# Optimization experiments

Hardware: AMD Instinct MI355X
Metric: run time of the kernel (lower is better)

Reference implementation:

```python
import jax, jax.numpy as jnp
import numpy as np

B, N, C = 8, 4096, 768
H, M = 12, 64          # num_heads, num_landmarks
D = C // H             # head_dim = 64


def setup_inputs() -> dict:
    key = jax.random.key(0)
    k1, k2, k3, k4 = jax.random.split(key, 4)
    s = 0.02
    return {
        "x": jax.random.normal(k1, (B, N, C), dtype=jnp.float32),
        "w_qkv": jax.random.normal(k2, (3 * C, C), dtype=jnp.float32) * s,
        "w_proj": jax.random.normal(k3, (C, C), dtype=jnp.float32) * s,
        "b_proj": jax.random.normal(k4, (C,), dtype=jnp.float32) * s,
    }


def iterative_inv(mat, n_iter=6):
    # mat: [B, H, M, M]; Newton-Schulz cubic iteration for pseudo-inverse
    I = jnp.eye(mat.shape[-1], dtype=mat.dtype)
    K = mat
    # init: K^T / max_j(sum_i K_ij)  per (B,H)
    scale = jnp.max(jnp.sum(K, axis=-2), axis=-1)[:, :, None, None]
    V = jnp.swapaxes(K, -1, -2) / scale
    for _ in range(n_iter):
        KV = K @ V
        V = 0.25 * V @ (13.0 * I - KV @ (15.0 * I - KV @ (7.0 * I - KV)))
    return V


def reference(x, w_qkv, w_proj, b_proj):
    b, n, c = x.shape
    qkv = (x @ w_qkv.T).reshape(b, n, 3, H, D).transpose(2, 0, 3, 1, 4)  # [3,B,H,N,D]
    Q, K, V = qkv[0], qkv[1], qkv[2]
    Q = Q / (D ** 0.5)
    # landmark pooling (N % M == 0 path): segment means of length N//M
    Kl = K.reshape(b, H, M, n // M, D).mean(axis=-2)  # [B,H,M,D]
    Ql = Q.reshape(b, H, M, n // M, D).mean(axis=-2)  # [B,H,M,D]
    kernel1 = jax.nn.softmax(jnp.einsum('bhnd,bhmd->bhnm', Q, Kl), axis=-1)   # [B,H,N,M]
    kernel2 = jax.nn.softmax(jnp.einsum('bhmd,bhld->bhml', Ql, Kl), axis=-1)  # [B,H,M,M]
    kernel3 = jax.nn.softmax(jnp.einsum('bhmd,bhnd->bhmn', Ql, K), axis=-1)   # [B,H,M,N]
    SV = (kernel1 @ iterative_inv(kernel2)) @ (kernel3 @ V)  # [B,H,N,D]
    SV = SV.transpose(0, 2, 1, 3).reshape(b, n, c)
    out = SV @ w_proj.T + b_proj
    out = out + V.transpose(0, 2, 1, 3).reshape(b, n, c)
    return out
```

## Files before the change

### kernel.cpp

```cpp
#include <hip/hip_runtime.h>
#include <hip/hip_bf16.h>
#include <stdint.h>

typedef __bf16 bf16;
typedef __bf16 bf16x8 __attribute__((ext_vector_type(8)));
typedef __bf16 bf16x4 __attribute__((ext_vector_type(4)));
typedef float f32x4 __attribute__((ext_vector_type(4)));

#define B_ 8
#define N_ 4096
#define C_ 768
#define H_ 12
#define M_ 64
#define D_ 64
#define NT_ 32768
#define C3_ 2304

typedef __attribute__((address_space(3))) void lds_void_t;
typedef const __attribute__((address_space(1))) void gvoid_t;

__device__ __forceinline__ void gl_lds16(const void* gsrc, void* ldst) {
  __builtin_amdgcn_global_load_lds((gvoid_t*)(uintptr_t)gsrc,
                                   (lds_void_t*)(uintptr_t)ldst, 16, 0, 0);
}

__device__ __forceinline__ f32x4 mfma16(bf16x8 a, bf16x8 b, f32x4 c) {
  return __builtin_amdgcn_mfma_f32_16x16x32_bf16(a, b, c, 0, 0, 0);
}

__global__ void k_cvt(const float* __restrict__ in, bf16* __restrict__ out, int n4) {
  const int stride = gridDim.x * blockDim.x;
  for (int i = blockIdx.x * blockDim.x + threadIdx.x; i < n4; i += stride) {
    f32x4 v = *(const f32x4*)(in + (size_t)i * 4);
    bf16x4 o;
    o[0] = (bf16)v[0]; o[1] = (bf16)v[1]; o[2] = (bf16)v[2]; o[3] = (bf16)v[3];
    *(bf16x4*)(out + (size_t)i * 4) = o;
  }
}

__global__ __launch_bounds__(256, 2) void k_qkv(
    const bf16* __restrict__ xbf, const bf16* __restrict__ wbf,
    bf16* __restrict__ Qb, bf16* __restrict__ Kb, bf16* __restrict__ Vb,
    float* __restrict__ Qlf, float* __restrict__ Klf)
{
  __shared__ bf16 As[2][128 * 32];
  __shared__ bf16 Bs[2][128 * 32];
  const int t = threadIdx.x;
  const int wave = t >> 6, lane = t & 63;
  const int bt = blockIdx.x & 255;
  const int ct = blockIdx.x >> 8;
  const int row0 = bt * 128, col0 = ct * 128;
  const int srow = t >> 2;
  const int scol = (t & 3) * 8;
  const bf16* ga = xbf + (size_t)row0 * C_ + scol;
  const bf16* gb = wbf + (size_t)col0 * C_ + scol;
  const int wr = wave >> 1, wc = wave & 1;

  f32x4 acc[4][4] = {};

#define QKV_STAGE(bi, k0)                                                      \
  {                                                                            \
    gl_lds16(ga + (size_t)srow * C_ + (k0), &As[bi][t * 8]);                   \
    gl_lds16(ga + (size_t)(srow + 64) * C_ + (k0), &As[bi][(t + 256) * 8]);    \
    gl_lds16(gb + (size_t)srow * C_ + (k0), &Bs[bi][t * 8]);                   \
    gl_lds16(gb + (size_t)(srow + 64) * C_ + (k0), &Bs[bi][(t + 256) * 8]);    \
  }

  QKV_STAGE(0, 0);
  __syncthreads();
  for (int ks = 0; ks < 24; ++ks) {
    const int buf = ks & 1;
    if (ks < 23) QKV_STAGE(buf ^ 1, (ks + 1) * 32);
    bf16x8 af[4], bfr[4];
#pragma unroll
    for (int i = 0; i < 4; ++i) {
      af[i]  = *(const bf16x8*)&As[buf][(wr * 64 + i * 16 + (lane & 15)) * 32 + 8 * (lane >> 4)];
      bfr[i] = *(const bf16x8*)&Bs[buf][(wc * 64 + i * 16 + (lane & 15)) * 32 + 8 * (lane >> 4)];
    }
#pragma unroll
    for (int i = 0; i < 4; ++i)
#pragma unroll
      for (int j = 0; j < 4; ++j)
        acc[i][j] = mfma16(af[i], bfr[j], acc[i][j]);
    __syncthreads();
  }
#undef QKV_STAGE

  const int colblock = col0 + wc * 64;
  const int which = colblock / C_;
  const int h = (colblock % C_) / D_;
  const int b = row0 >> 12;
  const int n_base = (row0 & (N_ - 1)) + wr * 64;
  bf16* dst = (which == 0) ? Qb : (which == 1) ? Kb : Vb;
  const float scale = (which == 0) ? 0.125f : 1.0f;
  const size_t base = ((size_t)(b * H_ + h) * N_ + n_base) * D_;
#pragma unroll
  for (int i = 0; i < 4; ++i)
#pragma unroll
    for (int q = 0; q < 4; ++q) {
      const int rloc = i * 16 + (lane >> 4) * 4 + q;
#pragma unroll
      for (int j = 0; j < 4; ++j) {
        const int d = j * 16 + (lane & 15);
        dst[base + (size_t)rloc * D_ + d] = (bf16)(acc[i][j][q] * scale);
      }
    }
  if (which < 2) {
    float* lmout = (which == 0) ? Qlf : Klf;
    const int m = n_base >> 6;
#pragma unroll
    for (int j = 0; j < 4; ++j) {
      float s = 0.f;
#pragma unroll
      for (int i = 0; i < 4; ++i)
#pragma unroll
        for (int q = 0; q < 4; ++q) s += acc[i][j][q];
      s *= scale;
      s += __shfl_xor(s, 16);
      s += __shfl_xor(s, 32);
      if ((lane >> 4) == 0)
        lmout[((size_t)(b * H_ + h) * M_ + m) * D_ + j * 16 + lane] = s * (1.0f / 64.0f);
    }
  }
}

__global__ __launch_bounds__(512, 1) void k_inv(
    const float* __restrict__ Qlf, const float* __restrict__ Klf,
    float* __restrict__ pinv)
{
  __shared__ float K2[4096];
  __shared__ float Vm[4096];
  __shared__ float KV[4096];
  __shared__ float T1[4096];
  __shared__ float U1[4096];
  __shared__ float tmp64[64];
  __shared__ float sscale;
  const int t = threadIdx.x;
  const int bh = blockIdx.x;
  const size_t off = (size_t)bh * 4096;
  for (int idx = t; idx < 4096; idx += 512) T1[idx] = Qlf[off + idx];
  for (int idx = t; idx < 4096; idx += 512) {
    const int r = idx >> 6, c = idx & 63;
    U1[c * 64 + r] = Klf[off + idx];
  }
  __syncthreads();
  const int j0 = (t & 15) * 4;
  const int i0 = (t >> 4) * 2;

  auto MMstep = [&](const float* A, const float* Bm, float* O, float dg, float sg, float al) {
    float r2[2][4] = {};
    for (int k = 0; k < 64; ++k) {
      f32x4 bv = *(const f32x4*)&Bm[k * 64 + j0];
      const float a0 = A[(i0 + 0) * 64 + k];
      const float a1 = A[(i0 + 1) * 64 + k];
#pragma unroll
      for (int jj = 0; jj < 4; ++jj) { r2[0][jj] += a0 * bv[jj]; r2[1][jj] += a1 * bv[jj]; }
    }
#pragma unroll
    for (int ii = 0; ii < 2; ++ii)
#pragma unroll
      for (int jj = 0; jj < 4; ++jj)
        O[(i0 + ii) * 64 + j0 + jj] = al * (dg * A[(i0 + ii) * 64 + (j0 + jj)] + sg * r2[ii][jj]);
    __syncthreads();
  };

  {
    float r2[2][4] = {};
    for (int k = 0; k < 64; ++k) {
      f32x4 bv = *(const f32x4*)&U1[k * 64 + j0];
      const float a0 = T1[(i0 + 0) * 64 + k];
      const float a1 = T1[(i0 + 1) * 64 + k];
#pragma unroll
      for (int jj = 0; jj < 4; ++jj) { r2[0][jj] += a0 * bv[jj]; r2[1][jj] += a1 * bv[jj]; }
    }
#pragma unroll
    for (int ii = 0; ii < 2; ++ii)
#pragma unroll
      for (int jj = 0; jj < 4; ++jj)
        K2[(i0 + ii) * 64 + j0 + jj] = __expf(r2[ii][jj]);
  }
  __syncthreads();
  if (t < 64) {
    float s = 0.f;
    for (int k = 0; k < 64; ++k) s += K2[t * 64 + k];
    tmp64[t] = 1.0f / s;
  }
  __syncthreads();
  for (int idx = t; idx < 4096; idx += 512) K2[idx] *= tmp64[idx >> 6];
  __syncthreads();
  if (t < 64) {
    float s = 0.f;
    for (int i = 0; i < 64; ++i) s += K2[i * 64 + t];
    tmp64[t] = s;
  }
  __syncthreads();
  if (t == 0) {
    float mx = tmp64[0];
    for (int j2 = 1; j2 < 64; ++j2) mx = fmaxf(mx, tmp64[j2]);
    sscale = 1.0f / mx;
  }
  __syncthreads();
  for (int idx = t; idx < 4096; idx += 512) {
    const int r = idx >> 6, c = idx & 63;
    Vm[idx] = K2[c * 64 + r] * sscale;
  }
  __syncthreads();

  float* pV = Vm;
  float* pT = T1;
  for (int it = 0; it < 6; ++it) {
    MMstep(K2, pV, KV, 0.f, 1.f, 1.f);
    MMstep(KV, KV, pT, 7.f, -1.f, 1.f);
    MMstep(KV, pT, U1, 15.f, -1.f, 1.f);
    MMstep(pV, U1, pT, 13.f, -1.f, 0.25f);
    float* sw = pV; pV = pT; pT = sw;
  }
  for (int idx = t; idx < 4096; idx += 512) pinv[off + idx] = pV[idx];
}

__global__ __launch_bounds__(256, 2) void k_k3v(
    const bf16* __restrict__ Qlb, const bf16* __restrict__ Kb, const bf16* __restrict__ Vb,
    float* __restrict__ Zacc, float* __restrict__ rowsum_g)
{
  __shared__ bf16 Qls[64 * 64];
  __shared__ bf16 Ks[128 * 64];
  __shared__ bf16 Vs[128 * 64];
  __shared__ bf16 Ps[64 * 128];
  __shared__ float rs[64];
  const int t = threadIdx.x, wave = t >> 6, lane = t & 63;
  const int bh = blockIdx.x >> 3;
  const int chunk = blockIdx.x & 7;
  const size_t kvbase = (size_t)bh * N_ * D_ + (size_t)chunk * 512 * D_;
  {
    const bf16* g = Qlb + (size_t)bh * 4096;
    gl_lds16(g + t * 8, &Qls[t * 8]);
    gl_lds16(g + (t + 256) * 8, &Qls[(t + 256) * 8]);
  }
  if (t < 64) rs[t] = 0.f;
  f32x4 z[4] = {};
  for (int st = 0; st < 4; ++st) {
    const bf16* gk = Kb + kvbase + (size_t)st * 128 * D_;
    const bf16* gv = Vb + kvbase + (size_t)st * 128 * D_;
#pragma unroll
    for (int c = 0; c < 4; ++c) {
      gl_lds16(gk + (t + c * 256) * 8, &Ks[(t + c * 256) * 8]);
      gl_lds16(gv + (t + c * 256) * 8, &Vs[(t + c * 256) * 8]);
    }
    __syncthreads();
    f32x4 sacc[4][2] = {};
#pragma unroll
    for (int kk = 0; kk < 2; ++kk) {
      bf16x8 af[4], bk[2];
#pragma unroll
      for (int i = 0; i < 4; ++i)
        af[i] = *(const bf16x8*)&Qls[(i * 16 + (lane & 15)) * 64 + kk * 32 + 8 * (lane >> 4)];
#pragma unroll
      for (int j2 = 0; j2 < 2; ++j2)
        bk[j2] = *(const bf16x8*)&Ks[(wave * 32 + j2 * 16 + (lane & 15)) * 64 + kk * 32 + 8 * (lane >> 4)];
#pragma unroll
      for (int i = 0; i < 4; ++i)
#pragma unroll
        for (int j2 = 0; j2 < 2; ++j2)
          sacc[i][j2] = mfma16(af[i], bk[j2], sacc[i][j2]);
    }
#pragma unroll
    for (int i = 0; i < 4; ++i)
#pragma unroll
      for (int q = 0; q < 4; ++q) {
        const float e0 = __expf(sacc[i][0][q]);
        const float e1 = __expf(sacc[i][1][q]);
        const int m = i * 16 + (lane >> 4) * 4 + q;
        Ps[m * 128 + wave * 32 + (lane & 15)] = (bf16)e0;
        Ps[m * 128 + wave * 32 + 16 + (lane & 15)] = (bf16)e1;
        float p = e0 + e1;
        p += __shfl_xor(p, 1); p += __shfl_xor(p, 2);
        p += __shfl_xor(p, 4); p += __shfl_xor(p, 8);
        if ((lane & 15) == 0) atomicAdd(&rs[m], p);
      }
    __syncthreads();
#pragma unroll
    for (int kk = 0; kk < 4; ++kk) {
      const int kbase = kk * 32 + 8 * (lane >> 4);
      const int d = wave * 16 + (lane & 15);
      bf16x8 bv;
#pragma unroll
      for (int e = 0; e < 8; ++e) bv[e] = Vs[(kbase + e) * 64 + d];
#pragma unroll
      for (int i = 0; i < 4; ++i) {
        bf16x8 ap = *(const bf16x8*)&Ps[(i * 16 + (lane & 15)) * 128 + kbase];
        z[i] = mfma16(ap, bv, z[i]);
      }
    }
    __syncthreads();
  }
  const size_t zbase = (size_t)bh * 4096;
#pragma unroll
  for (int i = 0; i < 4; ++i)
#pragma unroll
    for (int q = 0; q < 4; ++q) {
      const int m = i * 16 + (lane >> 4) * 4 + q;
      const int d = wave * 16 + (lane & 15);
      atomicAdd(&Zacc[zbase + m * 64 + d], z[i][q]);
    }
  if (t < 64) atomicAdd(&rowsum_g[bh * 64 + t], rs[t]);
}

__global__ __launch_bounds__(256, 1) void k_comb(
    const float* __restrict__ pinv, const float* __restrict__ Zacc,
    const float* __restrict__ rowsum_g, bf16* __restrict__ Wtb)
{
  __shared__ float Pv[4096];
  __shared__ float Zn[4096];
  const int t = threadIdx.x, bh = blockIdx.x;
  const size_t off = (size_t)bh * 4096;
  for (int idx = t; idx < 4096; idx += 256) Pv[idx] = pinv[off + idx];
  for (int idx = t; idx < 4096; idx += 256)
    Zn[idx] = Zacc[off + idx] / rowsum_g[bh * 64 + (idx >> 6)];
  __syncthreads();
  const int j0 = (t & 15) * 4, i0 = (t >> 4) * 4;
  float r[4][4] = {{0.f}};
  for (int k = 0; k < 64; ++k) {
    f32x4 bv = *(const f32x4*)&Zn[k * 64 + j0];
    float a[4];
#pragma unroll
    for (int ii = 0; ii < 4; ++ii) a[ii] = Pv[(i0 + ii) * 64 + k];
#pragma unroll
    for (int ii = 0; ii < 4; ++ii)
#pragma unroll
      for (int jj = 0; jj < 4; ++jj) r[ii][jj] += a[ii] * bv[jj];
  }
#pragma unroll
  for (int ii = 0; ii < 4; ++ii)
#pragma unroll
    for (int jj = 0; jj < 4; ++jj)
      Wtb[off + (size_t)(j0 + jj) * 64 + (i0 + ii)] = (bf16)r[ii][jj];
}

__global__ __launch_bounds__(256, 2) void k_sv(
    const bf16* __restrict__ Qb, const bf16* __restrict__ Klb,
    const bf16* __restrict__ Wtb, bf16* __restrict__ SVb)
{
  __shared__ bf16 Qs[128 * 64];
  __shared__ bf16 Kls[64 * 64];
  __shared__ bf16 Wts[64 * 64];
  __shared__ bf16 Ps[128 * 64];
  const int t = threadIdx.x, wave = t >> 6, lane = t & 63;
  const int bh = blockIdx.x >> 5;
  const int nt = blockIdx.x & 31;
  const int b = bh / H_, h = bh % H_;
  {
    const bf16* gq = Qb + (size_t)bh * N_ * D_ + (size_t)nt * 128 * D_;
#pragma unroll
    for (int c = 0; c < 4; ++c) gl_lds16(gq + (t + c * 256) * 8, &Qs[(t + c * 256) * 8]);
    const bf16* gkl = Klb + (size_t)bh * 4096;
    gl_lds16(gkl + t * 8, &Kls[t * 8]);
    gl_lds16(gkl + (t + 256) * 8, &Kls[(t + 256) * 8]);
    const bf16* gw = Wtb + (size_t)bh * 4096;
    gl_lds16(gw + t * 8, &Wts[t * 8]);
    gl_lds16(gw + (t + 256) * 8, &Wts[(t + 256) * 8]);
  }
  __syncthreads();
  f32x4 sacc[2][4] = {};
#pragma unroll
  for (int kk = 0; kk < 2; ++kk) {
    bf16x8 af[2], bl[4];
#pragma unroll
    for (int r = 0; r < 2; ++r)
      af[r] = *(const bf16x8*)&Qs[(wave * 32 + r * 16 + (lane & 15)) * 64 + kk * 32 + 8 * (lane >> 4)];
#pragma unroll
    for (int j = 0; j < 4; ++j)
      bl[j] = *(const bf16x8*)&Kls[(j * 16 + (lane & 15)) * 64 + kk * 32 + 8 * (lane >> 4)];
#pragma unroll
    for (int r = 0; r < 2; ++r)
#pragma unroll
      for (int j = 0; j < 4; ++j)
        sacc[r][j] = mfma16(af[r], bl[j], sacc[r][j]);
  }
#pragma unroll
  for (int r = 0; r < 2; ++r)
#pragma unroll
    for (int q = 0; q < 4; ++q) {
      float e[4]; float s = 0.f;
#pragma unroll
      for (int j = 0; j < 4; ++j) { e[j] = __expf(sacc[r][j][q]); s += e[j]; }
      s += __shfl_xor(s, 1); s += __shfl_xor(s, 2);
      s += __shfl_xor(s, 4); s += __shfl_xor(s, 8);
      const float is = 1.0f / s;
      const int row = wave * 32 + r * 16 + (lane >> 4) * 4 + q;
#pragma unroll
      for (int j = 0; j < 4; ++j)
        Ps[row * 64 + j * 16 + (lane & 15)] = (bf16)(e[j] * is);
    }
  __syncthreads();
  f32x4 oacc[2][4] = {};
#pragma unroll
  for (int kk = 0; kk < 2; ++kk) {
    bf16x8 af[2], bw[4];
#pragma unroll
    for (int r = 0; r < 2; ++r)
      af[r] = *(const bf16x8*)&Ps[(wave * 32 + r * 16 + (lane & 15)) * 64 + kk * 32 + 8 * (lane >> 4)];
#pragma unroll
    for (int j = 0; j < 4; ++j)
      bw[j] = *(const bf16x8*)&Wts[(j * 16 + (lane & 15)) * 64 + kk * 32 + 8 * (lane >> 4)];
#pragma unroll
    for (int r = 0; r < 2; ++r)
#pragma unroll
      for (int j = 0; j < 4; ++j)
        oacc[r][j] = mfma16(af[r], bw[j], oacc[r][j]);
  }
  const size_t outbase = ((size_t)b * N_ + (size_t)nt * 128) * C_ + h * 64;
#pragma unroll
  for (int r = 0; r < 2; ++r)
#pragma unroll
    for (int q = 0; q < 4; ++q) {
      const int row = wave * 32 + r * 16 + (lane >> 4) * 4 + q;
#pragma unroll
      for (int j = 0; j < 4; ++j)
        SVb[outbase + (size_t)row * C_ + j * 16 + (lane & 15)] = (bf16)(oacc[r][j][q]);
    }
}

__global__ __launch_bounds__(256, 2) void k_proj(
    const bf16* __restrict__ SVb, const bf16* __restrict__ wpb,
    const float* __restrict__ bproj, const bf16* __restrict__ Vb,
    float* __restrict__ outp)
{
  __shared__ bf16 As[2][128 * 32];
  __shared__ bf16 Bs[2][128 * 32];
  const int t = threadIdx.x;
  const int wave = t >> 6, lane = t & 63;
  const int bt = blockIdx.x & 255;
  const int ct = blockIdx.x >> 8;
  const int row0 = bt * 128, col0 = ct * 128;
  const int srow = t >> 2;
  const int scol = (t & 3) * 8;
  const bf16* ga = SVb + (size_t)row0 * C_ + scol;
  const bf16* gb = wpb + (size_t)col0 * C_ + scol;
  const int wr = wave >> 1, wc = wave & 1;

  f32x4 acc[4][4] = {};

#define PROJ_STAGE(bi, k0)                                                     \
  {                                                                            \
    gl_lds16(ga + (size_t)srow * C_ + (k0), &As[bi][t * 8]);                   \
    gl_lds16(ga + (size_t)(srow + 64) * C_ + (k0), &As[bi][(t + 256) * 8]);    \
    gl_lds16(gb + (size_t)srow * C_ + (k0), &Bs[bi][t * 8]);                   \
    gl_lds16(gb + (size_t)(srow + 64) * C_ + (k0), &Bs[bi][(t + 256) * 8]);    \
  }

  PROJ_STAGE(0, 0);
  __syncthreads();
  for (int ks = 0; ks < 24; ++ks) {
    const int buf = ks & 1;
    if (ks < 23) PROJ_STAGE(buf ^ 1, (ks + 1) * 32);
    bf16x8 af[4], bfr[4];
#pragma unroll
    for (int i = 0; i < 4; ++i) {
      af[i]  = *(const bf16x8*)&As[buf][(wr * 64 + i * 16 + (lane & 15)) * 32 + 8 * (lane >> 4)];
      bfr[i] = *(const bf16x8*)&Bs[buf][(wc * 64 + i * 16 + (lane & 15)) * 32 + 8 * (lane >> 4)];
    }
#pragma unroll
    for (int i = 0; i < 4; ++i)
#pragma unroll
      for (int j = 0; j < 4; ++j)
        acc[i][j] = mfma16(af[i], bfr[j], acc[i][j]);
    __syncthreads();
  }
#undef PROJ_STAGE

#pragma unroll
  for (int i = 0; i < 4; ++i)
#pragma unroll
    for (int q = 0; q < 4; ++q) {
      const int row = row0 + wr * 64 + i * 16 + (lane >> 4) * 4 + q;
      const int b = row >> 12, n = row & (N_ - 1);
#pragma unroll
      for (int j = 0; j < 4; ++j) {
        const int col = col0 + wc * 64 + j * 16 + (lane & 15);
        const int h = col >> 6, d = col & 63;
        const float v = acc[i][j][q] + bproj[col] +
                        (float)Vb[((size_t)(b * H_ + h) * N_ + n) * D_ + d];
        outp[(size_t)row * C_ + col] = v;
      }
    }
}

extern "C" void kernel_launch(void* const* d_in, const int* in_sizes, int n_in,
                              void* d_out, int out_size, void* d_ws, size_t ws_size,
                              hipStream_t stream) {
  const float* x = (const float*)d_in[0];
  const float* wqkv = (const float*)d_in[1];
  const float* wproj = (const float*)d_in[2];
  const float* bproj = (const float*)d_in[3];
  float* outp = (float*)d_out;
  char* ws = (char*)d_ws;

  size_t off = 0;
  auto take = [&](size_t bytes) { char* p = ws + off; off += bytes; return p; };
  bf16* xbf     = (bf16*)take(50331648);
  bf16* wqkvbf  = (bf16*)take(3538944);
  bf16* wprojbf = (bf16*)take(1179648);
  bf16* Qb      = (bf16*)take(50331648);
  bf16* Kb      = (bf16*)take(50331648);
  bf16* Vb      = (bf16*)take(50331648);
  float* Qlf    = (float*)take(1572864);
  float* Klf    = (float*)take(1572864);
  bf16* Qlb     = (bf16*)take(786432);
  bf16* Klb     = (bf16*)take(786432);
  float* pinvp  = (float*)take(1572864);
  float* Zacc   = (float*)take(1572864);
  float* rowsum = (float*)take(24576);
  bf16* Wtb     = (bf16*)take(786432);
  bf16* SVb     = xbf;

  hipMemsetAsync(Zacc, 0, 1572864 + 24576, stream);

  k_cvt<<<2048, 256, 0, stream>>>(x, xbf, 25165824 / 4);
  k_cvt<<<432, 256, 0, stream>>>(wqkv, wqkvbf, 1769472 / 4);
  k_cvt<<<144, 256, 0, stream>>>(wproj, wprojbf, 589824 / 4);
  k_qkv<<<256 * 18, 256, 0, stream>>>(xbf, wqkvbf, Qb, Kb, Vb, Qlf, Klf);
  k_cvt<<<96, 256, 0, stream>>>(Qlf, Qlb, 393216 / 4);
  k_cvt<<<96, 256, 0, stream>>>(Klf, Klb, 393216 / 4);
  k_inv<<<96, 512, 0, stream>>>(Qlf, Klf, pinvp);
  k_k3v<<<768, 256, 0, stream>>>(Qlb, Kb, Vb, Zacc, rowsum);
  k_comb<<<96, 256, 0, stream>>>(pinvp, Zacc, rowsum, Wtb);
  k_sv<<<96 * 32, 256, 0, stream>>>(Qb, Klb, Wtb, SVb);
  k_proj<<<256 * 6, 256, 0, stream>>>(SVb, wprojbf, bproj, Vb, outp);
}
```

Baseline: 428.7 us.

## Rework QKV GEMM into 256x256 tiles with 4-stage swizzled LDS pipeline

The QKV projection GEMM moves from 128x128 tiles with 4 waves and double buffering to 256x256 tiles with 8 waves, a 4-deep LDS ring fed by global_load_lds, and XOR-swizzled LDS addressing to cut bank conflicts. Block IDs are remapped for L2 locality, and the k-loop uses explicit vmcnt waits, barriers and setprio around the MFMA bursts so loads overlap compute. The larger tile raises arithmetic intensity and halves operand refetch. In exchange it uses much more LDS and registers per block, which lowers occupancy and makes the hand-written waitcnt schedule fragile.

```diff
diff --git a/kernel.cpp b/kernel.cpp
--- a/kernel.cpp
+++ b/kernel.cpp
@@ -38,88 +38,132 @@
   }
 }
 
-__global__ __launch_bounds__(256, 2) void k_qkv(
+__global__ __launch_bounds__(512, 2) void k_qkv(
     const bf16* __restrict__ xbf, const bf16* __restrict__ wbf,
     bf16* __restrict__ Qb, bf16* __restrict__ Kb, bf16* __restrict__ Vb,
     float* __restrict__ Qlf, float* __restrict__ Klf)
 {
-  __shared__ bf16 As[2][128 * 32];
-  __shared__ bf16 Bs[2][128 * 32];
+  __shared__ bf16 As[4][8192];
+  __shared__ bf16 Bs[4][8192];
   const int t = threadIdx.x;
   const int wave = t >> 6, lane = t & 63;
-  const int bt = blockIdx.x & 255;
-  const int ct = blockIdx.x >> 8;
-  const int row0 = bt * 128, col0 = ct * 128;
+  const int l15 = lane & 15, l16 = lane >> 4;
+
+  const int bid = blockIdx.x;
+  const int swz = (bid & 7) * 144 + (bid >> 3);
+  const int bt = swz / 9;
+  const int ct = swz % 9;
+  const int row0 = bt * 256, col0 = ct * 256;
+  const int wr = wave >> 2, wc = wave & 3;
+
   const int srow = t >> 2;
-  const int scol = (t & 3) * 8;
-  const bf16* ga = xbf + (size_t)row0 * C_ + scol;
-  const bf16* gb = wbf + (size_t)col0 * C_ + scol;
-  const int wr = wave >> 1, wc = wave & 1;
-
-  f32x4 acc[4][4] = {};
-
-#define QKV_STAGE(bi, k0)                                                      \
-  {                                                                            \
-    gl_lds16(ga + (size_t)srow * C_ + (k0), &As[bi][t * 8]);                   \
-    gl_lds16(ga + (size_t)(srow + 64) * C_ + (k0), &As[bi][(t + 256) * 8]);    \
-    gl_lds16(gb + (size_t)srow * C_ + (k0), &Bs[bi][t * 8]);                   \
-    gl_lds16(gb + (size_t)(srow + 64) * C_ + (k0), &Bs[bi][(t + 256) * 8]);    \
-  }
-
-  QKV_STAGE(0, 0);
-  __syncthreads();
-  for (int ks = 0; ks < 24; ++ks) {
-    const int buf = ks & 1;
-    if (ks < 23) QKV_STAGE(buf ^ 1, (ks + 1) * 32);
-    bf16x8 af[4], bfr[4];
-#pragma unroll
-    for (int i = 0; i < 4; ++i) {
-      af[i]  = *(const bf16x8*)&As[buf][(wr * 64 + i * 16 + (lane & 15)) * 32 + 8 * (lane >> 4)];
-      bfr[i] = *(const bf16x8*)&Bs[buf][(wc * 64 + i * 16 + (lane & 15)) * 32 + 8 * (lane >> 4)];
-    }
-#pragma unroll
-    for (int i = 0; i < 4; ++i)
-#pragma unroll
-      for (int j = 0; j < 4; ++j)
-        acc[i][j] = mfma16(af[i], bfr[j], acc[i][j]);
-    __syncthreads();
-  }
-#undef QKV_STAGE
+  const int scol = (((t & 3) ^ ((t >> 3) & 3)) << 3);
+  const bf16* gaBase = xbf + (size_t)(row0 + srow) * C_ + scol;
+  const bf16* gbBase = wbf + (size_t)(col0 + srow) * C_ + scol;
+
+  const int arow = wr * 128 + l15;
+  const int aoff = arow * 32 + ((l16 ^ ((l15 >> 1) & 3)) << 3);
+  const int brow = wc * 64 + l15;
+  const int boff = brow * 32 + ((l16 ^ ((l15 >> 1) & 3)) << 3);
+
+  f32x4 acc[8][4] = {};
+
+#define BAR() { __builtin_amdgcn_sched_barrier(0); __builtin_amdgcn_s_barrier(); __builtin_amdgcn_sched_barrier(0); }
+#define VMW8 asm volatile("s_waitcnt vmcnt(8)" ::: "memory")
+#define VMW4 asm volatile("s_waitcnt vmcnt(4)" ::: "memory")
+#define VMW0 asm volatile("s_waitcnt vmcnt(0)" ::: "memory")
+
+#define STAGE_HALF(kt3, c) {                                                     \
+    const int sb_ = (kt3) & 3;                                                   \
+    gl_lds16(gaBase + (size_t)((c) * 128) * C_ + (kt3) * 32,                     \
+             &As[sb_][(c) * 4096 + t * 8]);                                      \
+    gl_lds16(gbBase + (size_t)((c) * 128) * C_ + (kt3) * 32,                     \
+             &Bs[sb_][(c) * 4096 + t * 8]); }
+
+#define KSTEP(kt, DO_STAGE, VMW_) {                                              \
+    const bf16* as_ = As[(kt) & 3];                                              \
+    const bf16* bs_ = Bs[(kt) & 3];                                              \
+    if (DO_STAGE) STAGE_HALF((kt) + 3, 0);                                       \
+    bf16x8 bfr[4], afr[4];                                                       \
+    _Pragma("unroll")                                                            \
+    for (int j = 0; j < 4; ++j) bfr[j] = *(const bf16x8*)&bs_[boff + j * 512];   \
+    _Pragma("unroll")                                                            \
+    for (int i = 0; i < 4; ++i) afr[i] = *(const bf16x8*)&as_[aoff + i * 512];   \
+    BAR();                                                                       \
+    __builtin_amdgcn_s_setprio(1);                                               \
+    _Pragma("unroll")                                                            \
+    for (int i = 0; i < 4; ++i)                                                  \
+      _Pragma("unroll")                                                          \
+      for (int j = 0; j < 4; ++j)                                                \
+        acc[i][j] = mfma16(afr[i], bfr[j], acc[i][j]);                           \
+    __builtin_amdgcn_s_setprio(0);                                               \
+    BAR();                                                                       \
+    if (DO_STAGE) STAGE_HALF((kt) + 3, 1);                                       \
+    _Pragma("unroll")                                                            \
+    for (int i = 0; i < 4; ++i)                                                  \
+      afr[i] = *(const bf16x8*)&as_[aoff + (4 + i) * 512];                       \
+    BAR();                                                                       \
+    __builtin_amdgcn_s_setprio(1);                                               \
+    _Pragma("unroll")                                                            \
+    for (int i = 0; i < 4; ++i)                                                  \
+      _Pragma("unroll")                                                          \
+      for (int j = 0; j < 4; ++j)                                                \
+        acc[4 + i][j] = mfma16(afr[i], bfr[j], acc[4 + i][j]);                   \
+    __builtin_amdgcn_s_setprio(0);                                               \
+    VMW_;                                                                        \
+    BAR(); }
+
+  STAGE_HALF(0, 0); STAGE_HALF(0, 1);
+  STAGE_HALF(1, 0); STAGE_HALF(1, 1);
+  STAGE_HALF(2, 0); STAGE_HALF(2, 1);
+  VMW8;
+  BAR();
+
+  for (int kt = 0; kt < 21; ++kt) { KSTEP(kt, true, VMW8); }
+  KSTEP(21, false, VMW4);
+  KSTEP(22, false, VMW0);
+  KSTEP(23, false, (void)0);
+
+#undef KSTEP
+#undef STAGE_HALF
 
   const int colblock = col0 + wc * 64;
   const int which = colblock / C_;
   const int h = (colblock % C_) / D_;
   const int b = row0 >> 12;
-  const int n_base = (row0 & (N_ - 1)) + wr * 64;
+  const int n_base = (row0 & (N_ - 1)) + wr * 128;
   bf16* dst = (which == 0) ? Qb : (which == 1) ? Kb : Vb;
   const float scale = (which == 0) ? 0.125f : 1.0f;
   const size_t base = ((size_t)(b * H_ + h) * N_ + n_base) * D_;
 #pragma unroll
-  for (int i = 0; i < 4; ++i)
+  for (int i = 0; i < 8; ++i)
 #pragma unroll
     for (int q = 0; q < 4; ++q) {
-      const int rloc = i * 16 + (lane >> 4) * 4 + q;
+      const int rloc = i * 16 + l16 * 4 + q;
 #pragma unroll
       for (int j = 0; j < 4; ++j) {
-        const int d = j * 16 + (lane & 15);
+        const int d = j * 16 + l15;
         dst[base + (size_t)rloc * D_ + d] = (bf16)(acc[i][j][q] * scale);
       }
     }
   if (which < 2) {
     float* lmout = (which == 0) ? Qlf : Klf;
-    const int m = n_base >> 6;
-#pragma unroll
-    for (int j = 0; j < 4; ++j) {
-      float s = 0.f;
-#pragma unroll
-      for (int i = 0; i < 4; ++i)
-#pragma unroll
-        for (int q = 0; q < 4; ++q) s += acc[i][j][q];
-      s *= scale;
-      s += __shfl_xor(s, 16);
-      s += __shfl_xor(s, 32);
-      if ((lane >> 4) == 0)
-        lmout[((size_t)(b * H_ + h) * M_ + m) * D_ + j * 16 + lane] = s * (1.0f / 64.0f);
+#pragma unroll
+    for (int g = 0; g < 2; ++g) {
+      const int m = (n_base >> 6) + g;
+#pragma unroll
+      for (int j = 0; j < 4; ++j) {
+        float s = 0.f;
+#pragma unroll
+        for (int i = 4 * g; i < 4 * g + 4; ++i)
+#pragma unroll
+          for (int q = 0; q < 4; ++q) s += acc[i][j][q];
+        s *= scale;
+        s += __shfl_xor(s, 16);
+        s += __shfl_xor(s, 32);
+        if (l16 == 0)
+          lmout[((size_t)(b * H_ + h) * M_ + m) * D_ + j * 16 + lane] = s * (1.0f / 64.0f);
+      }
     }
   }
 }
@@ -518,7 +562,7 @@
   k_cvt<<<2048, 256, 0, stream>>>(x, xbf, 25165824 / 4);
   k_cvt<<<432, 256, 0, stream>>>(wqkv, wqkvbf, 1769472 / 4);
   k_cvt<<<144, 256, 0, stream>>>(wproj, wprojbf, 589824 / 4);
-  k_qkv<<<256 * 18, 256, 0, stream>>>(xbf, wqkvbf, Qb, Kb, Vb, Qlf, Klf);
+  k_qkv<<<1152, 512, 0, stream>>>(xbf, wqkvbf, Qb, Kb, Vb, Qlf, Klf);
   k_cvt<<<96, 256, 0, stream>>>(Qlf, Qlb, 393216 / 4);
   k_cvt<<<96, 256, 0, stream>>>(Klf, Klb, 393216 / 4);
   k_inv<<<96, 512, 0, stream>>>(Qlf, Klf, pinvp);
```

Result: faster. 409.6 us (-4.5%).
